# Performance work log

Hardware: AMD Instinct MI355X
Metric: run time of the kernel (lower is better)

## Reference

```python
import jax, jax.numpy as jnp
import numpy as np

PERIOD = 15          # hardcoded in the torch module's forward: STL(series, 15)
N_SEASONAL = 7       # statsmodels STL default seasonal smoother length
N_TREND = 29         # smallest odd >= 1.5*p/(1-1.5/7) = 28.64 -> 29 (statsmodels default)
N_LOWPASS = 17       # smallest odd > period (statsmodels default)
N_INNER = 2          # statsmodels: robust=False -> 2 inner iterations, 0 outer


def _loess_matrix(n, q, ts):
    """Dense linear operator for degree-1 LOESS smoothing of a length-n series
    evaluated at (possibly out-of-range) integer positions ts. Non-robust LOESS is
    linear in y, so smoothing == matmul with this constant matrix."""
    M = np.zeros((len(ts), n), dtype=np.float64)
    qq = min(q, n)
    for i, t in enumerate(ts):
        left = int(np.clip(t - (q - 1) // 2, 0, n - qq))
        right = left + qq - 1
        h = max(t - left, right - t)
        if q > n:
            h += (q - n) / 2.0
        xs = np.arange(left, right + 1, dtype=np.float64)
        w = np.clip(1.0 - (np.abs(xs - t) / h) ** 3, 0.0, None) ** 3  # tricube
        w = w / w.sum()
        xbar = (w * xs).sum()
        var = (w * (xs - xbar) ** 2).sum()
        a = w.copy()
        if var > 1e-12:  # degree-1 local linear fit; fall back to deg-0 if degenerate
            a = w * (1.0 + (t - xbar) * (xs - xbar) / var)
        M[i, left:right + 1] = a
    return M.astype(np.float32)


def _ma(x, k):
    """Moving average of window k along last axis (valid mode)."""
    cs = jnp.cumsum(x, axis=-1)
    cs = jnp.concatenate([jnp.zeros(x.shape[:-1] + (1,), x.dtype), cs], axis=-1)
    return (cs[..., k:] - cs[..., :-k]) / k


def setup_inputs() -> dict:
    key = jax.random.key(0)
    x = jax.random.normal(key, (128, 480, 256), dtype=jnp.float32)  # [B, T, C]
    return {"x": x}


def reference(x):
    B, T, Cc = x.shape
    p = PERIOD
    n_sub = T // p  # cycle-subseries length; T chosen divisible by period

    # Constant LOESS smoothing operators (numpy, baked in as jit constants)
    M_seas = jnp.asarray(_loess_matrix(n_sub, N_SEASONAL, np.arange(-1, n_sub + 1)))  # (n_sub+2, n_sub)
    M_lp = jnp.asarray(_loess_matrix(T, N_LOWPASS, np.arange(T)))                     # (T, T)
    M_trend = jnp.asarray(_loess_matrix(T, N_TREND, np.arange(T)))                    # (T, T)

    y = jnp.transpose(x, (0, 2, 1))  # [B, C, T]
    trend = jnp.zeros_like(y)
    seasonal = jnp.zeros_like(y)

    for _ in range(N_INNER):  # STL inner loop (Cleveland 1990, non-robust)
        # 1. detrend
        D = y - trend
        # 2. cycle-subseries LOESS smoothing, extended one period each side
        Dsub = D.reshape(B, Cc, n_sub, p)                      # subseries along axis 2
        Cext = jnp.einsum('sn,bcnp->bcsp', M_seas, Dsub)       # [B,C,n_sub+2,p]
        Cext = Cext.reshape(B, Cc, (n_sub + 2) * p)            # time order, length T+2p
        # 3. low-pass: MA(p) x2, MA(3), then LOESS(n_l)
        lp = _ma(_ma(_ma(Cext, p), p), 3)                      # length T
        L = jnp.einsum('tn,bcn->bct', M_lp, lp)
        # 4. seasonal = smoothed subseries (center T) minus low-pass
        seasonal = Cext[..., p:p + T] - L
        # 5+6. deseasonalize and trend LOESS
        trend = jnp.einsum('tn,bcn->bct', M_trend, y - seasonal)

    resid = y - seasonal - trend
    seas_plus_resid = jnp.transpose(seasonal + resid, (0, 2, 1))  # [B, T, C]
    trend_out = jnp.transpose(trend, (0, 2, 1))
    return (seas_plus_resid, trend_out)
```

## Files before the change

### kernel.cpp

```cpp
#include <hip/hip_runtime.h>
#include <hip/hip_bf16.h>
#include <stdint.h>

#define TLEN 480
#define NB 128
#define NC 256

typedef short bf16x8 __attribute__((ext_vector_type(8)));
typedef float f32x4 __attribute__((ext_vector_type(4)));
typedef unsigned short u16;
typedef unsigned int u32;

__device__ inline u16 f2bf(float f) {
    union { float f; uint32_t u; } v; v.f = f;
    uint32_t u = v.u;
    return (u16)((u + 0x7fffu + ((u >> 16) & 1u)) >> 16);
}

__device__ inline u32 pack2bf(float lo, float hi) {
    return __builtin_amdgcn_perm(__float_as_uint(hi), __float_as_uint(lo), 0x07060302u);
}

template<int N, int Q>
__device__ __forceinline__ int loess_wT(int t, float* out) {
    int left = t - (Q - 1) / 2;
    if (left < 0) left = 0;
    if (left > N - Q) left = N - Q;
    int right = left + Q - 1;
    int h = (t - left) > (right - t) ? (t - left) : (right - t);
    double w[Q];
    double wsum = 0.0;
    #pragma unroll
    for (int i = 0; i < Q; ++i) {
        double dist = fabs((double)(left + i - t)) / (double)h;
        double u = 1.0 - dist * dist * dist;
        if (u < 0.0) u = 0.0;
        double wv = u * u * u;
        w[i] = wv; wsum += wv;
    }
    #pragma unroll
    for (int i = 0; i < Q; ++i) w[i] /= wsum;
    double xbar = 0.0;
    #pragma unroll
    for (int i = 0; i < Q; ++i) xbar += w[i] * (double)(left + i);
    double var = 0.0;
    #pragma unroll
    for (int i = 0; i < Q; ++i) { double d = (double)(left + i) - xbar; var += w[i] * d * d; }
    if (var > 1e-12) {
        double tb = (double)t - xbar;
        #pragma unroll
        for (int i = 0; i < Q; ++i) {
            double d = (double)(left + i) - xbar;
            out[i] = (float)(w[i] * (1.0 + tb * d / var));
        }
    } else {
        #pragma unroll
        for (int i = 0; i < Q; ++i) out[i] = (float)w[i];
    }
    return left;
}

__global__ void k_loess(float* Ms, float* w3, float* MlpC, float* MtC) {
    int gid = blockIdx.x * 256 + threadIdx.x;
    if (gid < 34) {
        float wl[7];
        int left = loess_wT<32, 7>(gid - 1, wl);
        float* row = Ms + gid * 32;
        #pragma unroll
        for (int i = 0; i < 32; ++i) row[i] = 0.0f;
        #pragma unroll
        for (int i = 0; i < 7; ++i) row[left + i] = wl[i];
    } else if (gid < 514) {
        int t = gid - 34;
        float wl[17];
        loess_wT<TLEN, 17>(t, wl);
        #pragma unroll
        for (int i = 0; i < 17; ++i) MlpC[t * 17 + i] = wl[i];
    } else if (gid < 994) {
        int t = gid - 514;
        float wl[29];
        loess_wT<TLEN, 29>(t, wl);
        #pragma unroll
        for (int i = 0; i < 29; ++i) MtC[t * 29 + i] = wl[i];
    } else if (gid < 1025) {
        int d = gid - 994;
        int cnt = 0;
        for (int c = 0; c < 3; ++c)
            for (int a = 0; a < 15; ++a) {
                int b = d - a - c;
                if (b >= 0 && b < 15) cnt++;
            }
        w3[d] = (float)((double)cnt / 675.0);
    }
}

__global__ void k_S(const float* __restrict__ Ms, const float* __restrict__ w3,
                    const float* __restrict__ MlpC, float* __restrict__ S) {
    int id = blockIdx.x * 256 + threadIdx.x;
    if (id >= TLEN * TLEN) return;
    int t = id / TLEN, u = id - t * TLEN;
    int nu = u / 15, ju = u - nu * 15;
    int slp = t - 8;
    if (slp < 0) slp = 0;
    if (slp > TLEN - 17) slp = TLEN - 17;
    float acc = 0.0f;
    for (int k = 0; k < 17; ++k) {
        int i = slp + k;
        int s_lo = (i - ju + 14) / 15;
        float g = 0.0f;
        #pragma unroll
        for (int ds = 0; ds < 3; ++ds) {
            int s = s_lo + ds;
            int d = s * 15 + ju - i;
            if (s >= 0 && s < 34 && d >= 0 && d <= 30)
                g += Ms[s * 32 + nu] * w3[d];
        }
        acc += MlpC[t * 17 + k] * g;
    }
    float val = -acc;
    if (t % 15 == ju) val += Ms[(1 + t / 15) * 32 + nu];
    S[id] = val;
}

__global__ void k_VU(const float* __restrict__ MtC, const float* __restrict__ S,
                     float* __restrict__ U, float* __restrict__ V) {
    int id = blockIdx.x * 256 + threadIdx.x;
    if (id >= TLEN * TLEN) return;
    int t = id / TLEN, u = id - t * TLEN;
    int st = t - 14;
    if (st < 0) st = 0;
    if (st > TLEN - 29) st = TLEN - 29;
    float acc = 0.0f;
    for (int k = 0; k < 29; ++k)
        acc += MtC[t * 29 + k] * S[(size_t)(st + k) * TLEN + u];
    float mt = (u >= st && u < st + 29) ? MtC[t * 29 + (u - st)] : 0.0f;
    V[id] = acc;
    U[id] = mt - acc;
}

__global__ void k_A(const float* __restrict__ U, const float* __restrict__ V,
                    u16* __restrict__ Abf) {
    __shared__ float Vs[16][17];
    __shared__ float Us[16][17];
    int tx = threadIdx.x, ty = threadIdx.y;
    int u = blockIdx.x * 16 + tx;
    int t = blockIdx.y * 16 + ty;
    float acc = 0.0f;
    for (int kt = 0; kt < 30; ++kt) {
        Vs[ty][tx] = V[(size_t)t * TLEN + kt * 16 + tx];
        Us[ty][tx] = U[(size_t)(kt * 16 + ty) * TLEN + u];
        __syncthreads();
        #pragma unroll
        for (int e = 0; e < 16; ++e) acc += Vs[ty][e] * Us[e][tx];
        __syncthreads();
    }
    Abf[(size_t)t * TLEN + u] = f2bf(U[(size_t)t * TLEN + u] + acc);
}

__global__ __launch_bounds__(256, 5)
void k_gemm(const u16* __restrict__ A, const float* __restrict__ x,
            float* __restrict__ out0, float* __restrict__ out1) {
    __shared__ u16 Xs[32 * 488];
    int b = blockIdx.x;
    int t0 = blockIdx.y * 96;
    int cz = blockIdx.z * 32;
    int tid = threadIdx.x;
    int wave = tid >> 6, lane = tid & 63;
    int lane15 = lane & 15, quad = lane >> 4;
    int wt = wave & 1, wc = wave >> 1;

    int cq  = tid & 7;
    int kq0 = tid >> 3;
    const float* xp0 = x + (size_t)b * TLEN * NC + (size_t)(kq0 * 4) * NC + cz + cq * 4;
    u32* l32 = (u32*)Xs;
    int lbase = (cq * 4) * 244 + kq0 * 2;

    float4 ra[4], rb[4];
    {
        #pragma unroll
        for (int q = 0; q < 4; ++q) ra[q] = *(const float4*)(xp0 + q * NC);
    }
    #pragma unroll
    for (int p = 0; p < 4; ++p) {
        float4* cur = (p & 1) ? rb : ra;
        float4* nxt = (p & 1) ? ra : rb;
        if (p < 3) {
            if (p + 1 < 3 || kq0 < 24) {
                const float* xp = xp0 + (size_t)(p + 1) * 128 * NC;
                #pragma unroll
                for (int q = 0; q < 4; ++q) nxt[q] = *(const float4*)(xp + q * NC);
            }
        }
        if (p < 3 || kq0 < 24) {
            const float* fl = (const float*)cur;
            int o = lbase + p * 64;
            #pragma unroll
            for (int cc = 0; cc < 4; ++cc) {
                uint2 w;
                w.x = pack2bf(fl[0 * 4 + cc], fl[1 * 4 + cc]);
                w.y = pack2bf(fl[2 * 4 + cc], fl[3 * 4 + cc]);
                *(uint2*)(l32 + o + cc * 244) = w;
            }
        }
    }
    __syncthreads();

    const u16* bp0 = A + (size_t)(t0 + wt * 48 + lane15) * TLEN + quad * 8;
    int arow = (wc * 16 + lane15) * 488 + quad * 8;

    f32x4 acc[3] = {};
    bf16x8 bcur[3], bnxt[3], acur, anxt;
    #pragma unroll
    for (int j = 0; j < 3; ++j) bcur[j] = *(const bf16x8*)(bp0 + (size_t)j * 16 * TLEN);
    acur = *(const bf16x8*)&Xs[arow];

    #pragma unroll
    for (int s = 0; s < 15; ++s) {
        bf16x8* bc = (s & 1) ? bnxt : bcur;
        bf16x8* bn = (s & 1) ? bcur : bnxt;
        bf16x8& ac = (s & 1) ? anxt : acur;
        bf16x8& an = (s & 1) ? acur : anxt;
        if (s < 14) {
            int k = (s + 1) * 32;
            #pragma unroll
            for (int j = 0; j < 3; ++j)
                bn[j] = *(const bf16x8*)(bp0 + (size_t)j * 16 * TLEN + k);
            an = *(const bf16x8*)&Xs[arow + k];
        }
        #pragma unroll
        for (int j = 0; j < 3; ++j)
            acc[j] = __builtin_amdgcn_mfma_f32_16x16x32_bf16(ac, bc[j], acc[j], 0, 0, 0);
    }

    __syncthreads();

    float* T = (float*)Xs;
    float* R = T + 96 * 36;
    #pragma unroll
    for (int j = 0; j < 3; ++j) {
        int tl = wt * 48 + j * 16 + lane15;
        int clb = wc * 16 + quad * 4;
        f32x4 tv = acc[j];
        size_t gb = ((size_t)b * TLEN + t0 + tl) * NC + cz + clb;
        f32x4 xv = *(const f32x4*)(x + gb);
        *(f32x4*)&T[tl * 36 + clb] = tv;
        *(f32x4*)&R[tl * 36 + clb] = xv - tv;
    }
    __syncthreads();

    #pragma unroll
    for (int v = 0; v < 3; ++v) {
        int id = v * 256 + tid;
        int tl = id >> 3, c4 = (id & 7) * 4;
        size_t gb = ((size_t)b * TLEN + t0 + tl) * NC + cz + c4;
        f32x4 tv = *(const f32x4*)&T[tl * 36 + c4];
        f32x4 rv = *(const f32x4*)&R[tl * 36 + c4];
        __builtin_nontemporal_store(tv, (f32x4*)(out1 + gb));
        __builtin_nontemporal_store(rv, (f32x4*)(out0 + gb));
    }
}

extern "C" void kernel_launch(void* const* d_in, const int* in_sizes, int n_in,
                              void* d_out, int out_size, void* d_ws, size_t ws_size,
                              hipStream_t stream) {
    const float* x = (const float*)d_in[0];
    float* out0 = (float*)d_out;
    float* out1 = (float*)d_out + (size_t)NB * TLEN * NC;

    char* ws = (char*)d_ws;
    size_t oMs  = 0;
    size_t oW3  = oMs + 4352;
    size_t oLpC = oW3 + 128;
    size_t oMtC = oLpC + 32640;
    size_t oS   = oMtC + 55680;
    size_t oU   = oS + 921600;
    size_t oV   = oU + 921600;
    size_t oA   = oV + 921600;

    float* Ms   = (float*)(ws + oMs);
    float* w3   = (float*)(ws + oW3);
    float* MlpC = (float*)(ws + oLpC);
    float* MtC  = (float*)(ws + oMtC);
    float* S    = (float*)(ws + oS);
    float* U    = (float*)(ws + oU);
    float* V    = (float*)(ws + oV);
    u16*   Abf  = (u16*)(ws + oA);

    k_loess<<<5, 256, 0, stream>>>(Ms, w3, MlpC, MtC);
    k_S<<<900, 256, 0, stream>>>(Ms, w3, MlpC, S);
    k_VU<<<900, 256, 0, stream>>>(MtC, S, U, V);
    k_A<<<dim3(30, 30), dim3(16, 16), 0, stream>>>(U, V, Abf);
    k_gemm<<<dim3(NB, 5, 8), 256, 0, stream>>>(Abf, x, out0, out1);
}
```

Baseline: 278.8 us.

## Pre-transpose input to bf16 buffer and widen GEMM channel tile to 64

Adds a separate kernel that converts x to bf16 and transposes it to [B,C,T] in workspace once. The GEMM then reads its A operand directly from global memory instead of staging through shared memory. The channel tile per block is doubled to 64, so each wave computes 2x3 MFMA tiles. Before, each of the five t-blocks re-read and converted the full x slab. This removes that redundant read and the LDS staging, at the cost of an extra kernel launch plus a write and read of a bf16 copy of x.

```diff
diff --git a/kernel.cpp b/kernel.cpp
--- a/kernel.cpp
+++ b/kernel.cpp
@@ -8,6 +8,7 @@
 
 typedef short bf16x8 __attribute__((ext_vector_type(8)));
 typedef float f32x4 __attribute__((ext_vector_type(4)));
+typedef unsigned int u32x4 __attribute__((ext_vector_type(4)));
 typedef unsigned short u16;
 typedef unsigned int u32;
 
@@ -91,6 +92,54 @@
                 if (b >= 0 && b < 15) cnt++;
             }
         w3[d] = (float)((double)cnt / 675.0);
+    }
+}
+
+__global__ __launch_bounds__(256, 2)
+void k_T(const float* __restrict__ x, u16* __restrict__ xT) {
+    __shared__ u16 Xs[64 * 488];
+    int b = blockIdx.x;
+    int cz = blockIdx.y * 64;
+    int tid = threadIdx.x;
+    int wq = tid & 15, kkq = tid >> 4;
+    const float* xp0 = x + (size_t)b * TLEN * NC + (size_t)(kkq * 4) * NC + cz + wq * 4;
+    u32* l32 = (u32*)Xs;
+    int lbase = (wq * 4) * 244 + kkq * 2;
+
+    float4 ra[4], rb[4];
+    #pragma unroll
+    for (int q = 0; q < 4; ++q) ra[q] = *(const float4*)(xp0 + q * NC);
+    #pragma unroll
+    for (int p = 0; p < 8; ++p) {
+        float4* cur = (p & 1) ? rb : ra;
+        float4* nxt = (p & 1) ? ra : rb;
+        if (p < 7) {
+            if (p + 1 < 7 || kkq < 8) {
+                const float* xp = xp0 + (size_t)(p + 1) * 64 * NC;
+                #pragma unroll
+                for (int q = 0; q < 4; ++q) nxt[q] = *(const float4*)(xp + q * NC);
+            }
+        }
+        if (p < 7 || kkq < 8) {
+            const float* fl = (const float*)cur;
+            int o = lbase + p * 32;
+            #pragma unroll
+            for (int cc = 0; cc < 4; ++cc) {
+                uint2 w;
+                w.x = pack2bf(fl[0 * 4 + cc], fl[1 * 4 + cc]);
+                w.y = pack2bf(fl[2 * 4 + cc], fl[3 * 4 + cc]);
+                *(uint2*)(l32 + o + cc * 244) = w;
+            }
+        }
+    }
+    __syncthreads();
+
+    u16* dst = xT + ((size_t)b * NC + cz) * TLEN;
+    #pragma unroll
+    for (int v = 0; v < 15; ++v) {
+        int id = v * 256 + tid;
+        int c = id / 60, j = id - c * 60;
+        *(u32x4*)(dst + (size_t)c * TLEN + j * 8) = *(const u32x4*)&Xs[c * 488 + j * 8];
     }
 }
 
@@ -157,106 +206,69 @@
     Abf[(size_t)t * TLEN + u] = f2bf(U[(size_t)t * TLEN + u] + acc);
 }
 
-__global__ __launch_bounds__(256, 5)
-void k_gemm(const u16* __restrict__ A, const float* __restrict__ x,
+__global__ __launch_bounds__(256, 3)
+void k_gemm(const u16* __restrict__ A, const u16* __restrict__ xT,
+            const float* __restrict__ x,
             float* __restrict__ out0, float* __restrict__ out1) {
-    __shared__ u16 Xs[32 * 488];
+    __shared__ float T[96 * 68];
     int b = blockIdx.x;
     int t0 = blockIdx.y * 96;
-    int cz = blockIdx.z * 32;
+    int cz = blockIdx.z * 64;
     int tid = threadIdx.x;
     int wave = tid >> 6, lane = tid & 63;
     int lane15 = lane & 15, quad = lane >> 4;
-    int wt = wave & 1, wc = wave >> 1;
-
-    int cq  = tid & 7;
-    int kq0 = tid >> 3;
-    const float* xp0 = x + (size_t)b * TLEN * NC + (size_t)(kq0 * 4) * NC + cz + cq * 4;
-    u32* l32 = (u32*)Xs;
-    int lbase = (cq * 4) * 244 + kq0 * 2;
-
-    float4 ra[4], rb[4];
-    {
-        #pragma unroll
-        for (int q = 0; q < 4; ++q) ra[q] = *(const float4*)(xp0 + q * NC);
-    }
-    #pragma unroll
-    for (int p = 0; p < 4; ++p) {
-        float4* cur = (p & 1) ? rb : ra;
-        float4* nxt = (p & 1) ? ra : rb;
-        if (p < 3) {
-            if (p + 1 < 3 || kq0 < 24) {
-                const float* xp = xp0 + (size_t)(p + 1) * 128 * NC;
-                #pragma unroll
-                for (int q = 0; q < 4; ++q) nxt[q] = *(const float4*)(xp + q * NC);
-            }
-        }
-        if (p < 3 || kq0 < 24) {
-            const float* fl = (const float*)cur;
-            int o = lbase + p * 64;
-            #pragma unroll
-            for (int cc = 0; cc < 4; ++cc) {
-                uint2 w;
-                w.x = pack2bf(fl[0 * 4 + cc], fl[1 * 4 + cc]);
-                w.y = pack2bf(fl[2 * 4 + cc], fl[3 * 4 + cc]);
-                *(uint2*)(l32 + o + cc * 244) = w;
-            }
-        }
-    }
-    __syncthreads();
-
+    int wc = wave & 1, wt = wave >> 1;
+
+    const u16* ap0 = xT + ((size_t)b * NC + cz + wc * 32 + lane15) * TLEN + quad * 8;
     const u16* bp0 = A + (size_t)(t0 + wt * 48 + lane15) * TLEN + quad * 8;
-    int arow = (wc * 16 + lane15) * 488 + quad * 8;
-
-    f32x4 acc[3] = {};
-    bf16x8 bcur[3], bnxt[3], acur, anxt;
+
+    f32x4 acc[2][3] = {};
+    bf16x8 acur[2], anxt[2], bcur[3], bnxt[3];
+    acur[0] = *(const bf16x8*)ap0;
+    acur[1] = *(const bf16x8*)(ap0 + 16 * TLEN);
     #pragma unroll
     for (int j = 0; j < 3; ++j) bcur[j] = *(const bf16x8*)(bp0 + (size_t)j * 16 * TLEN);
-    acur = *(const bf16x8*)&Xs[arow];
 
     #pragma unroll
     for (int s = 0; s < 15; ++s) {
+        bf16x8* ac = (s & 1) ? anxt : acur;
+        bf16x8* an = (s & 1) ? acur : anxt;
         bf16x8* bc = (s & 1) ? bnxt : bcur;
         bf16x8* bn = (s & 1) ? bcur : bnxt;
-        bf16x8& ac = (s & 1) ? anxt : acur;
-        bf16x8& an = (s & 1) ? acur : anxt;
         if (s < 14) {
             int k = (s + 1) * 32;
+            an[0] = *(const bf16x8*)(ap0 + k);
+            an[1] = *(const bf16x8*)(ap0 + 16 * TLEN + k);
             #pragma unroll
             for (int j = 0; j < 3; ++j)
                 bn[j] = *(const bf16x8*)(bp0 + (size_t)j * 16 * TLEN + k);
-            an = *(const bf16x8*)&Xs[arow + k];
-        }
-        #pragma unroll
-        for (int j = 0; j < 3; ++j)
-            acc[j] = __builtin_amdgcn_mfma_f32_16x16x32_bf16(ac, bc[j], acc[j], 0, 0, 0);
-    }
-
+        }
+        #pragma unroll
+        for (int j = 0; j < 3; ++j) {
+            acc[0][j] = __builtin_amdgcn_mfma_f32_16x16x32_bf16(ac[0], bc[j], acc[0][j], 0, 0, 0);
+            acc[1][j] = __builtin_amdgcn_mfma_f32_16x16x32_bf16(ac[1], bc[j], acc[1][j], 0, 0, 0);
+        }
+    }
+
+    #pragma unroll
+    for (int i = 0; i < 2; ++i)
+        #pragma unroll
+        for (int j = 0; j < 3; ++j) {
+            int tl = wt * 48 + j * 16 + lane15;
+            int cl = wc * 32 + i * 16 + quad * 4;
+            *(f32x4*)&T[tl * 68 + cl] = acc[i][j];
+        }
     __syncthreads();
 
-    float* T = (float*)Xs;
-    float* R = T + 96 * 36;
-    #pragma unroll
-    for (int j = 0; j < 3; ++j) {
-        int tl = wt * 48 + j * 16 + lane15;
-        int clb = wc * 16 + quad * 4;
-        f32x4 tv = acc[j];
-        size_t gb = ((size_t)b * TLEN + t0 + tl) * NC + cz + clb;
+    #pragma unroll
+    for (int v = 0; v < 6; ++v) {
+        int id = v * 256 + tid;
+        int tl = id >> 4, c4 = (id & 15) * 4;
+        size_t gb = ((size_t)b * TLEN + t0 + tl) * NC + cz + c4;
+        f32x4 tv = *(const f32x4*)&T[tl * 68 + c4];
         f32x4 xv = *(const f32x4*)(x + gb);
-        *(f32x4*)&T[tl * 36 + clb] = tv;
-        *(f32x4*)&R[tl * 36 + clb] = xv - tv;
-    }
-    __syncthreads();
-
-    #pragma unroll
-    for (int v = 0; v < 3; ++v) {
-        int id = v * 256 + tid;
-        int tl = id >> 3, c4 = (id & 7) * 4;
-        size_t gb = ((size_t)b * TLEN + t0 + tl) * NC + cz + c4;
-        f32x4 tv = *(const f32x4*)&T[tl * 36 + c4];
-        f32x4 rv = *(const f32x4*)&R[tl * 36 + c4];
         __builtin_nontemporal_store(tv, (f32x4*)(out1 + gb));
-        __builtin_nontemporal_store(rv, (f32x4*)(out0 + gb));
+        __builtin_nontemporal_store(xv - tv, (f32x4*)(out0 + gb));
     }
 }
 
@@ -276,6 +288,7 @@
     size_t oU   = oS + 921600;
     size_t oV   = oU + 921600;
     size_t oA   = oV + 921600;
+    size_t oXT  = oA + 460800;
 
     float* Ms   = (float*)(ws + oMs);
     float* w3   = (float*)(ws + oW3);
@@ -285,10 +298,12 @@
     float* U    = (float*)(ws + oU);
     float* V    = (float*)(ws + oV);
     u16*   Abf  = (u16*)(ws + oA);
+    u16*   xT   = (u16*)(ws + oXT);
 
     k_loess<<<5, 256, 0, stream>>>(Ms, w3, MlpC, MtC);
+    k_T<<<dim3(NB, 4), 256, 0, stream>>>(x, xT);
     k_S<<<900, 256, 0, stream>>>(Ms, w3, MlpC, S);
     k_VU<<<900, 256, 0, stream>>>(MtC, S, U, V);
     k_A<<<dim3(30, 30), dim3(16, 16), 0, stream>>>(U, V, Abf);
-    k_gemm<<<dim3(NB, 5, 8), 256, 0, stream>>>(Abf, x, out0, out1);
-}
+    k_gemm<<<dim3(NB, 5, 4), 256, 0, stream>>>(Abf, xT, x, out0, out1);
+}
```

Result: no change. 277.8 us (-0.4%).
